# Performance work log

Hardware: AMD Instinct MI355X
Metric: run time of the kernel (lower is better)

## Reference

```python
import jax, jax.numpy as jnp
import numpy as np

N, E, F_IN, HID, NUM_CLASSES = 10000, 160000, 512, 1024, 100
NEG_SLOPE = 0.2  # PyG GATv2Conv default negative_slope


def setup_inputs() -> dict:
    key = jax.random.key(0)
    ks = jax.random.split(key, 10)
    return {
        "x": jax.random.normal(ks[0], (N, F_IN), jnp.float32),
        "edge_index": jax.random.randint(ks[1], (2, E), 0, N, dtype=jnp.int64)
        if jax.config.jax_enable_x64 else jax.random.randint(ks[1], (2, E), 0, N, dtype=jnp.int32),
        # GATv2Conv params (single head, out=1024): lin_l (source), lin_r (target), attention vector a, output bias
        "Wl": jax.random.normal(ks[2], (F_IN, HID), jnp.float32) / np.sqrt(F_IN),
        "bl": jnp.zeros((HID,), jnp.float32),
        "Wr": jax.random.normal(ks[3], (F_IN, HID), jnp.float32) / np.sqrt(F_IN),
        "br": jnp.zeros((HID,), jnp.float32),
        "att": jax.random.normal(ks[4], (HID,), jnp.float32) / np.sqrt(HID),
        "conv_b": jnp.zeros((HID,), jnp.float32),
        # MLP head: 1024 -> 512 -> 128 -> num_classes
        "W1": jax.random.normal(ks[5], (HID, 512), jnp.float32) / np.sqrt(HID),
        "b1": jnp.zeros((512,), jnp.float32),
        "W2": jax.random.normal(ks[6], (512, 128), jnp.float32) / np.sqrt(512),
        "b2": jnp.zeros((128,), jnp.float32),
        "Wc": jax.random.normal(ks[7], (128, NUM_CLASSES), jnp.float32) / np.sqrt(128),
        "bc": jnp.zeros((NUM_CLASSES,), jnp.float32),
    }


def _gatv2_conv(x, edge_index, Wl, bl, Wr, br, att, conv_b):
    """GATv2Conv, heads=1, add_self_loops=True, share_weights=False."""
    n = x.shape[0]
    loops = jnp.arange(n, dtype=edge_index.dtype)
    src = jnp.concatenate([edge_index[0], loops])  # message sources j
    dst = jnp.concatenate([edge_index[1], loops])  # message targets i
    xl = x @ Wl + bl  # [N, HID] source transform
    xr = x @ Wr + br  # [N, HID] target transform
    # e_ij = a^T LeakyReLU(xl_j + xr_i), per edge
    e = jax.nn.leaky_relu(xl[src] + xr[dst], negative_slope=NEG_SLOPE) @ att  # [E+N]
    # segment softmax over incoming edges of each target node (self-loops guarantee non-empty segments)
    m = jax.ops.segment_max(e, dst, num_segments=n)
    w = jnp.exp(e - m[dst])
    s = jax.ops.segment_sum(w, dst, num_segments=n)
    alpha = w / s[dst]  # [E+N]
    out = jax.ops.segment_sum(alpha[:, None] * xl[src], dst, num_segments=n)  # [N, HID]
    return out + conv_b


def reference(x, edge_index, Wl, bl, Wr, br, att, conv_b, W1, b1, W2, b2, Wc, bc):
    h = jax.nn.relu(_gatv2_conv(x, edge_index, Wl, bl, Wr, br, att, conv_b))
    h = jax.nn.relu(h @ W1 + b1)
    h = jax.nn.relu(h @ W2 + b2)
    return h @ Wc + bc
```

## Files before the change

### kernel.cpp

```cpp
#include <hip/hip_runtime.h>
#include <hip/hip_bf16.h>

constexpr int N_NODES = 10000;
constexpr int E_EDGES = 160000;
constexpr int F_IN    = 512;
constexpr int HID     = 1024;
constexpr int NCLS    = 100;
constexpr float NEG_SLOPE = 0.2f;

constexpr int BM = 128, BN = 128, BK = 32;
constexpr int M_PAD = ((N_NODES + BM - 1) / BM) * BM;

typedef __attribute__((ext_vector_type(8))) short bf16x8;
typedef __attribute__((ext_vector_type(4))) float f32x4;

__device__ inline void load_lds_16(const void* g, void* l) {
    __builtin_amdgcn_global_load_lds(
        (const __attribute__((address_space(1))) void*)g,
        (__attribute__((address_space(3))) void*)l, 16, 0, 0);
}

__device__ inline float bf2f(short s) {
    unsigned u = ((unsigned)(unsigned short)s) << 16;
    return __builtin_bit_cast(float, u);
}

__device__ inline float rfl(float x) {
    return __builtin_bit_cast(float,
        __builtin_amdgcn_readfirstlane(__builtin_bit_cast(int, x)));
}

__global__ __launch_bounds__(256) void gemm_mfma(
    const __hip_bfloat16* __restrict__ A, const __hip_bfloat16* __restrict__ Bt,
    const float* __restrict__ bias, int M, int K, int relu, int n_valid,
    __hip_bfloat16* __restrict__ Cb, int ldb, int m_blocks,
    const int* __restrict__ ei, int* __restrict__ cur, int* __restrict__ srcs)
{
    const int tid  = threadIdx.x;

    if ((int)blockIdx.y >= m_blocks) {
        int idx = ((blockIdx.y - m_blocks) * gridDim.x + blockIdx.x) * 256 + tid;
        if (idx < E_EDGES + N_NODES) {
            int s, d;
            if (idx < E_EDGES) { s = ei[idx]; d = ei[E_EDGES + idx]; }
            else               { s = idx - E_EDGES; d = s; }
            int p = atomicAdd(&cur[d], 1);
            srcs[p] = s;
        }
        return;
    }

    __shared__ __align__(16) short As[BM * BK];
    __shared__ __align__(16) short Bs[BN * BK];

    const int lane = tid & 63;
    const int w    = tid >> 6;
    const int m0   = blockIdx.y * BM;
    const int n0   = blockIdx.x * BN;

    f32x4 acc[4][4] = {};

    const int c0 = tid, c1 = tid + 256;
    const int r0 = c0 >> 2, cc0 = c0 & 3;
    const int r1 = c1 >> 2, cc1 = c1 & 3;

    const short* Ag0 = (const short*)A + (size_t)(m0 + r0) * K + cc0 * 8;
    const short* Ag1 = (const short*)A + (size_t)(m0 + r1) * K + cc1 * 8;
    const short* Bg0 = (const short*)Bt + (size_t)(n0 + r0) * K + cc0 * 8;
    const short* Bg1 = (const short*)Bt + (size_t)(n0 + r1) * K + cc1 * 8;

    const int wm = (w >> 1) * 64;
    const int wn = (w & 1) * 64;
    const int q  = lane >> 4;
    const int mr = lane & 15;

    for (int k0 = 0; k0 < K; k0 += BK) {
        __syncthreads();
        load_lds_16(Ag0 + k0, As + c0 * 8);
        load_lds_16(Ag1 + k0, As + c1 * 8);
        load_lds_16(Bg0 + k0, Bs + c0 * 8);
        load_lds_16(Bg1 + k0, Bs + c1 * 8);
        __syncthreads();

        bf16x8 af[4], bf[4];
        #pragma unroll
        for (int mt = 0; mt < 4; ++mt)
            af[mt] = *(const bf16x8*)&As[(wm + mt * 16 + mr) * BK + q * 8];
        #pragma unroll
        for (int nt = 0; nt < 4; ++nt)
            bf[nt] = *(const bf16x8*)&Bs[(wn + nt * 16 + mr) * BK + q * 8];
        #pragma unroll
        for (int mt = 0; mt < 4; ++mt)
            #pragma unroll
            for (int nt = 0; nt < 4; ++nt)
                acc[mt][nt] = __builtin_amdgcn_mfma_f32_16x16x32_bf16(
                    af[mt], bf[nt], acc[mt][nt], 0, 0, 0);
    }

    #pragma unroll
    for (int mt = 0; mt < 4; ++mt) {
        #pragma unroll
        for (int nt = 0; nt < 4; ++nt) {
            #pragma unroll
            for (int r = 0; r < 4; ++r) {
                int gm = m0 + wm + mt * 16 + q * 4 + r;
                int gn = n0 + wn + nt * 16 + mr;
                if (gm < M && gn < n_valid) {
                    float v = acc[mt][nt][r] + bias[gn];
                    if (relu) v = fmaxf(v, 0.f);
                    Cb[(size_t)gm * ldb + gn] = __float2bfloat16(v);
                }
            }
        }
    }
}

constexpr int HS_LD = 136;

__global__ __launch_bounds__(256) void mlp_tail(
    const __hip_bfloat16* __restrict__ h1, const __hip_bfloat16* __restrict__ W2t,
    const float* __restrict__ b2, const __hip_bfloat16* __restrict__ Wct,
    const float* __restrict__ bc, float* __restrict__ out)
{
    __shared__ __align__(16) short As[BM * BK];
    __shared__ __align__(16) short Bs[BN * BK];
    __shared__ __align__(16) short Hs[128 * HS_LD];

    const int tid  = threadIdx.x;
    const int lane = tid & 63;
    const int w    = tid >> 6;
    const int m0   = blockIdx.x * BM;

    const int c0 = tid, c1 = tid + 256;
    const int r0 = c0 >> 2, cc0 = c0 & 3;
    const int r1 = c1 >> 2, cc1 = c1 & 3;

    const int wm = (w >> 1) * 64;
    const int wn = (w & 1) * 64;
    const int q  = lane >> 4;
    const int mr = lane & 15;

    {
        f32x4 acc[4][4] = {};
        const short* Ag0 = (const short*)h1 + (size_t)(m0 + r0) * 512 + cc0 * 8;
        const short* Ag1 = (const short*)h1 + (size_t)(m0 + r1) * 512 + cc1 * 8;
        const short* Bg0 = (const short*)W2t + (size_t)r0 * 512 + cc0 * 8;
        const short* Bg1 = (const short*)W2t + (size_t)r1 * 512 + cc1 * 8;

        for (int k0 = 0; k0 < 512; k0 += BK) {
            __syncthreads();
            load_lds_16(Ag0 + k0, As + c0 * 8);
            load_lds_16(Ag1 + k0, As + c1 * 8);
            load_lds_16(Bg0 + k0, Bs + c0 * 8);
            load_lds_16(Bg1 + k0, Bs + c1 * 8);
            __syncthreads();

            bf16x8 af[4], bf[4];
            #pragma unroll
            for (int mt = 0; mt < 4; ++mt)
                af[mt] = *(const bf16x8*)&As[(wm + mt * 16 + mr) * BK + q * 8];
            #pragma unroll
            for (int nt = 0; nt < 4; ++nt)
                bf[nt] = *(const bf16x8*)&Bs[(wn + nt * 16 + mr) * BK + q * 8];
            #pragma unroll
            for (int mt = 0; mt < 4; ++mt)
                #pragma unroll
                for (int nt = 0; nt < 4; ++nt)
                    acc[mt][nt] = __builtin_amdgcn_mfma_f32_16x16x32_bf16(
                        af[mt], bf[nt], acc[mt][nt], 0, 0, 0);
        }
        #pragma unroll
        for (int mt = 0; mt < 4; ++mt)
            #pragma unroll
            for (int nt = 0; nt < 4; ++nt)
                #pragma unroll
                for (int r = 0; r < 4; ++r) {
                    int ml = wm + mt * 16 + q * 4 + r;
                    int nl = wn + nt * 16 + mr;
                    float v = fmaxf(acc[mt][nt][r] + b2[nl], 0.f);
                    Hs[ml * HS_LD + nl] =
                        __builtin_bit_cast(short, __float2bfloat16(v));
                }
    }

    {
        f32x4 acc[4][4] = {};
        const short* Bg0 = (const short*)Wct + (size_t)r0 * 128 + cc0 * 8;
        const short* Bg1 = (const short*)Wct + (size_t)r1 * 128 + cc1 * 8;

        for (int k0 = 0; k0 < 128; k0 += BK) {
            __syncthreads();
            load_lds_16(Bg0 + k0, Bs + c0 * 8);
            load_lds_16(Bg1 + k0, Bs + c1 * 8);
            __syncthreads();

            bf16x8 af[4], bf[4];
            #pragma unroll
            for (int mt = 0; mt < 4; ++mt)
                af[mt] = *(const bf16x8*)&Hs[(wm + mt * 16 + mr) * HS_LD + k0 + q * 8];
            #pragma unroll
            for (int nt = 0; nt < 4; ++nt)
                bf[nt] = *(const bf16x8*)&Bs[(wn + nt * 16 + mr) * BK + q * 8];
            #pragma unroll
            for (int mt = 0; mt < 4; ++mt)
                #pragma unroll
                for (int nt = 0; nt < 4; ++nt)
                    acc[mt][nt] = __builtin_amdgcn_mfma_f32_16x16x32_bf16(
                        af[mt], bf[nt], acc[mt][nt], 0, 0, 0);
        }
        #pragma unroll
        for (int mt = 0; mt < 4; ++mt)
            #pragma unroll
            for (int nt = 0; nt < 4; ++nt)
                #pragma unroll
                for (int r = 0; r < 4; ++r) {
                    int gm = m0 + wm + mt * 16 + q * 4 + r;
                    int gn = wn + nt * 16 + mr;
                    if (gm < N_NODES && gn < NCLS)
                        out[(size_t)gm * NCLS + gn] = acc[mt][nt][r] + bc[gn];
                }
    }
}

__device__ void transpose_tile(const float* __restrict__ W,
                               __hip_bfloat16* __restrict__ Wt,
                               int K, int N, int NP, int bx, int by,
                               int tx, int ty, float (*t)[33])
{
    int n0 = bx * 32, k0 = by * 32;
    #pragma unroll
    for (int i = 0; i < 32; i += 8) {
        int k = k0 + ty + i, n = n0 + tx;
        t[ty + i][tx] = (k < K && n < N) ? W[(size_t)k * N + n] : 0.f;
    }
    __syncthreads();
    #pragma unroll
    for (int i = 0; i < 32; i += 8) {
        int n = n0 + ty + i, k = k0 + tx;
        if (n < NP && k < K)
            Wt[(size_t)n * K + k] = __float2bfloat16(t[tx][ty + i]);
    }
}

constexpr int PK_X    = M_PAD * F_IN / 1024;
constexpr int PK_WL   = PK_X + 512;
constexpr int PK_WR   = PK_WL + 512;
constexpr int PK_W1   = PK_WR + 512;
constexpr int PK_W2   = PK_W1 + 64;
constexpr int PK_WC   = PK_W2 + 16;
constexpr int PK_BLR  = PK_WC + 8;
constexpr int PK_HIST = PK_BLR + (E_EDGES + 255) / 256;

__global__ __launch_bounds__(256) void pack_all(
    const float* __restrict__ x, __hip_bfloat16* __restrict__ xb,
    const float* __restrict__ Wl, const float* __restrict__ Wr,
    __hip_bfloat16* __restrict__ Wlrt,
    const float* __restrict__ W1, __hip_bfloat16* __restrict__ W1t,
    const float* __restrict__ W2, __hip_bfloat16* __restrict__ W2t,
    const float* __restrict__ Wc, __hip_bfloat16* __restrict__ Wct,
    const float* __restrict__ bl, const float* __restrict__ br,
    float* __restrict__ blr,
    const int* __restrict__ ei, int* __restrict__ deg)
{
    __shared__ float t[32][33];
    const int b = blockIdx.x;
    const int tid = threadIdx.x;
    const int tx = tid & 31, ty = tid >> 5;

    if (b < PK_X) {
        int i = b * 256 + tid;
        int row = i >> 7;
        int base = i << 2;
        short4 o;
        if (row < N_NODES) {
            const float4 v = *(const float4*)(x + base);
            o.x = __builtin_bit_cast(short, __float2bfloat16(v.x));
            o.y = __builtin_bit_cast(short, __float2bfloat16(v.y));
            o.z = __builtin_bit_cast(short, __float2bfloat16(v.z));
            o.w = __builtin_bit_cast(short, __float2bfloat16(v.w));
        } else {
            o.x = o.y = o.z = o.w = 0;
        }
        *(short4*)((short*)xb + base) = o;
    } else if (b < PK_WL) {
        int l = b - PK_X;
        transpose_tile(Wl, Wlrt, F_IN, HID, HID, l & 31, l >> 5, tx, ty, t);
    } else if (b < PK_WR) {
        int l = b - PK_WL;
        transpose_tile(Wr, Wlrt + (size_t)HID * F_IN, F_IN, HID, HID,
                       l & 31, l >> 5, tx, ty, t);
    } else if (b < PK_W1) {
        int l = b - PK_WR;
        transpose_tile(W1, W1t, HID, 512, 512, l & 15, l >> 4, tx, ty, t);
    } else if (b < PK_W2) {
        int l = b - PK_W1;
        transpose_tile(W2, W2t, 512, 128, 128, l & 3, l >> 2, tx, ty, t);
    } else if (b < PK_WC) {
        int l = b - PK_W2;
        transpose_tile(Wc, Wct, 128, NCLS, 128, l & 3, l >> 2, tx, ty, t);
    } else if (b < PK_BLR) {
        int i = (b - PK_WC) * 256 + tid;
        if (i < HID) blr[i] = bl[i];
        else if (i < 2 * HID) blr[i] = br[i - HID];
    } else {
        int e = (b - PK_BLR) * 256 + tid;
        if (e < E_EDGES) atomicAdd(&deg[ei[E_EDGES + e]], 1);
    }
}

__global__ __launch_bounds__(1024) void scan_deg(const int* __restrict__ deg,
                                                 int* __restrict__ off,
                                                 int* __restrict__ cur)
{
    __shared__ int tmp[1024];
    const int t = threadIdx.x;
    const int base = t * 10;
    int loc[10];
    int s = 0;
    #pragma unroll
    for (int j = 0; j < 10; ++j) {
        int n = base + j;
        loc[j] = s;
        s += (n < N_NODES) ? deg[n] + 1 : 0;
    }
    tmp[t] = s;
    __syncthreads();
    for (int st = 1; st < 1024; st <<= 1) {
        int add = (t >= st) ? tmp[t - st] : 0;
        __syncthreads();
        tmp[t] += add;
        __syncthreads();
    }
    const int excl = tmp[t] - s;
    #pragma unroll
    for (int j = 0; j < 10; ++j) {
        int n = base + j;
        if (n < N_NODES) { off[n] = excl + loc[j]; cur[n] = excl + loc[j]; }
    }
    if (t == 1023) off[N_NODES] = tmp[1023];
}

__global__ __launch_bounds__(256) void gat_node(
    const __hip_bfloat16* __restrict__ xlr, const float* __restrict__ att,
    const float* __restrict__ conv_b,
    const int* __restrict__ off, const int* __restrict__ srcs,
    __hip_bfloat16* __restrict__ h)
{
    const int tid  = threadIdx.x;
    const int lane = tid & 63;
    const int wave = tid >> 6;
    const int nloc = wave >> 1;
    const int wsub = wave & 1;
    const int i    = blockIdx.x * 2 + nloc;

    __shared__ float O_s[2][16 * 64];
    __shared__ float ml_s[2][2];

    const int beg  = off[i];
    const int end  = off[i + 1];
    const int last = end - 1;
    const short* base = (const short*)xlr;

    float xr_v[16], att_v[16];
    {
        const short* xri = base + (size_t)i * 2048 + HID + lane * 16;
        bf16x8 a0 = *(const bf16x8*)xri;
        bf16x8 a1 = *(const bf16x8*)(xri + 8);
        const float* ai = att + lane * 16;
        #pragma unroll
        for (int j = 0; j < 8; ++j) {
            xr_v[j] = bf2f(a0[j]);
            xr_v[8 + j] = bf2f(a1[j]);
        }
        #pragma unroll
        for (int j = 0; j < 16; ++j) att_v[j] = ai[j];
    }

    float m_w = -3e38f, l_w = 0.f;
    float O[16];
    #pragma unroll
    for (int j = 0; j < 16; ++j) O[j] = 0.f;

    int pos = beg + wsub;
    if (pos < end) {
        int sc = __builtin_amdgcn_readfirstlane(srcs[pos]);
        int sn = __builtin_amdgcn_readfirstlane(
                     srcs[pos + 2 <= last ? pos + 2 : last]);
        const short* rp = base + (size_t)sc * 2048 + lane * 16;
        bf16x8 a0 = *(const bf16x8*)rp;
        bf16x8 a1 = *(const bf16x8*)(rp + 8);

        for (; pos < end; pos += 2) {
            const short* np = base + (size_t)sn * 2048 + lane * 16;
            bf16x8 b0 = *(const bf16x8*)np;
            bf16x8 b1 = *(const bf16x8*)(np + 8);
            int s2 = srcs[pos + 4 <= last ? pos + 4 : last];

            float xf[16];
            #pragma unroll
            for (int j = 0; j < 8; ++j) {
                xf[j] = bf2f(a0[j]);
                xf[8 + j] = bf2f(a1[j]);
            }

            float p = 0.f;
            #pragma unroll
            for (int j = 0; j < 16; ++j) {
                float a = xf[j] + xr_v[j];
                a = fmaxf(a, NEG_SLOPE * a);
                p = __builtin_fmaf(att_v[j], a, p);
            }
            #pragma unroll
            for (int s = 1; s < 64; s <<= 1) p += __shfl_xor(p, s, 64);
            p = rfl(p);

            if (p > m_w) {
                const float scale = __expf(m_w - p);
                l_w = l_w * scale + 1.f;
                #pragma unroll
                for (int j = 0; j < 16; ++j) O[j] = O[j] * scale + xf[j];
                m_w = p;
            } else {
                const float alpha = __expf(p - m_w);
                l_w += alpha;
                #pragma unroll
                for (int j = 0; j < 16; ++j)
                    O[j] = __builtin_fmaf(alpha, xf[j], O[j]);
            }

            a0 = b0; a1 = b1;
            sn = __builtin_amdgcn_readfirstlane(s2);
        }
    }

    if (wsub == 1) {
        #pragma unroll
        for (int j = 0; j < 16; ++j) O_s[nloc][j * 64 + lane] = O[j];
        if (lane == 0) { ml_s[nloc][0] = m_w; ml_s[nloc][1] = l_w; }
    }
    __syncthreads();

    if (wsub == 0) {
        const float m1 = ml_s[nloc][0], l1 = ml_s[nloc][1];
        const float M  = fmaxf(m_w, m1);
        const float c0 = __expf(m_w - M);
        const float c1 = __expf(m1 - M);
        const float invL = 1.f / (l_w * c0 + l1 * c1);
        const float* cb = conv_b + lane * 16;
        bf16x8 o0, o1;
        #pragma unroll
        for (int j = 0; j < 8; ++j) {
            float r0 = __builtin_fmaf(
                c0 * O[j] + c1 * O_s[nloc][j * 64 + lane], invL, cb[j]);
            float r1 = __builtin_fmaf(
                c0 * O[8 + j] + c1 * O_s[nloc][(8 + j) * 64 + lane], invL,
                cb[8 + j]);
            r0 = fmaxf(r0, 0.f);
            r1 = fmaxf(r1, 0.f);
            o0[j] = __builtin_bit_cast(short, __float2bfloat16(r0));
            o1[j] = __builtin_bit_cast(short, __float2bfloat16(r1));
        }
        short* hp = (short*)h + (size_t)i * HID + lane * 16;
        *(bf16x8*)hp = o0;
        *(bf16x8*)(hp + 8) = o1;
    }
}

extern "C" void kernel_launch(void* const* d_in, const int* in_sizes, int n_in,
                              void* d_out, int out_size, void* d_ws, size_t ws_size,
                              hipStream_t stream)
{
    const float* x      = (const float*)d_in[0];
    const int*   ei     = (const int*)d_in[1];
    const float* Wl     = (const float*)d_in[2];
    const float* bl     = (const float*)d_in[3];
    const float* Wr     = (const float*)d_in[4];
    const float* br     = (const float*)d_in[5];
    const float* att    = (const float*)d_in[6];
    const float* conv_b = (const float*)d_in[7];
    const float* W1     = (const float*)d_in[8];
    const float* b1     = (const float*)d_in[9];
    const float* W2     = (const float*)d_in[10];
    const float* b2     = (const float*)d_in[11];
    const float* Wc     = (const float*)d_in[12];
    const float* bc     = (const float*)d_in[13];
    float* out = (float*)d_out;

    char* p = (char*)d_ws;
    __hip_bfloat16* xlr = (__hip_bfloat16*)p; p += (size_t)M_PAD * 2048 * 2;
    __hip_bfloat16* hb  = (__hip_bfloat16*)p; p += (size_t)M_PAD * HID * 2;
    __hip_bfloat16* xb  = (__hip_bfloat16*)p; p += (size_t)M_PAD * F_IN * 2;
    __hip_bfloat16* Wlrt= (__hip_bfloat16*)p; p += (size_t)2 * HID * F_IN * 2;
    __hip_bfloat16* W1t = (__hip_bfloat16*)p; p += (size_t)512 * HID * 2;
    __hip_bfloat16* W2t = (__hip_bfloat16*)p; p += (size_t)128 * 512 * 2;
    __hip_bfloat16* Wct = (__hip_bfloat16*)p; p += (size_t)128 * 128 * 2;
    float* blr = (float*)p;               p += 2 * HID * 4;
    int* deg  = (int*)p;                  p += N_NODES * 4;
    int* off  = (int*)p;                  p += (N_NODES + 1) * 4;
    int* cur  = (int*)p;                  p += N_NODES * 4;
    int* srcs = (int*)p;

    __hip_bfloat16* h1 = xb;

    const dim3 blk(256);

    hipMemsetAsync(deg, 0, N_NODES * sizeof(int), stream);

    pack_all<<<PK_HIST, blk, 0, stream>>>(x, xb, Wl, Wr, Wlrt, W1, W1t,
                                          W2, W2t, Wc, Wct, bl, br, blr,
                                          ei, deg);

    scan_deg<<<1, 1024, 0, stream>>>(deg, off, cur);

    constexpr int SCAT_Y = (E_EDGES + N_NODES + 16 * 256 - 1) / (16 * 256);
    gemm_mfma<<<dim3(2 * HID / BN, M_PAD / BM + SCAT_Y), blk, 0, stream>>>(
        xb, Wlrt, blr, N_NODES, F_IN, 0, 2 * HID, xlr, 2048,
        M_PAD / BM, ei, cur, srcs);

    gat_node<<<N_NODES / 2, blk, 0, stream>>>(xlr, att, conv_b, off, srcs, hb);

    gemm_mfma<<<dim3(512 / BN, M_PAD / BM), blk, 0, stream>>>(
        hb, W1t, b1, N_NODES, HID, 1, 512, h1, 512,
        M_PAD / BM, nullptr, nullptr, nullptr);

    mlp_tail<<<M_PAD / BM, blk, 0, stream>>>(h1, W2t, b2, Wct, bc, out);
}
```

Baseline: 277.8 us.

## Double-buffer LDS tiles, swizzle LDS layout, and vectorize GEMM epilogue stores

The main GEMM loop and the first stage of mlp_tail now use two LDS buffers. The next K-tile is prefetched with global_load_lds while the current tile feeds the MFMAs, which removes one barrier per iteration. The 16-byte chunk index in LDS is XOR-swizzled by row to cut bank conflicts on the fragment reads. The MFMA operands are swapped so each lane holds four consecutive columns, letting the epilogue write bias-added values as short4/float4 vector stores instead of scalar stores. With one barrier per iteration, correctness depends on the loads into the other buffer being ordered against the previous iteration's reads.

```diff
diff --git a/kernel.cpp b/kernel.cpp
--- a/kernel.cpp
+++ b/kernel.cpp
@@ -30,11 +30,25 @@
         __builtin_amdgcn_readfirstlane(__builtin_bit_cast(int, x)));
 }
 
+__device__ inline short4 cvt4(const f32x4 v, const float4 b, int relu) {
+    float r0 = v[0] + b.x, r1 = v[1] + b.y, r2 = v[2] + b.z, r3 = v[3] + b.w;
+    if (relu) {
+        r0 = fmaxf(r0, 0.f); r1 = fmaxf(r1, 0.f);
+        r2 = fmaxf(r2, 0.f); r3 = fmaxf(r3, 0.f);
+    }
+    short4 o;
+    o.x = __builtin_bit_cast(short, __float2bfloat16(r0));
+    o.y = __builtin_bit_cast(short, __float2bfloat16(r1));
+    o.z = __builtin_bit_cast(short, __float2bfloat16(r2));
+    o.w = __builtin_bit_cast(short, __float2bfloat16(r3));
+    return o;
+}
+
 __global__ __launch_bounds__(256) void gemm_mfma(
     const __hip_bfloat16* __restrict__ A, const __hip_bfloat16* __restrict__ Bt,
     const float* __restrict__ bias, int M, int K, int relu, int n_valid,
     __hip_bfloat16* __restrict__ Cb, int ldb, int m_blocks,
-    const int* __restrict__ ei, int* __restrict__ cur, int* __restrict__ srcs)
+    const int* __restrict__ ei, int* __restrict__ cur_, int* __restrict__ srcs)
 {
     const int tid  = threadIdx.x;
 
@@ -44,14 +58,14 @@
             int s, d;
             if (idx < E_EDGES) { s = ei[idx]; d = ei[E_EDGES + idx]; }
             else               { s = idx - E_EDGES; d = s; }
-            int p = atomicAdd(&cur[d], 1);
+            int p = atomicAdd(&cur_[d], 1);
             srcs[p] = s;
         }
         return;
     }
 
-    __shared__ __align__(16) short As[BM * BK];
-    __shared__ __align__(16) short Bs[BN * BK];
+    __shared__ __align__(16) short As[2][BM * BK];
+    __shared__ __align__(16) short Bs[2][BN * BK];
 
     const int lane = tid & 63;
     const int w    = tid >> 6;
@@ -61,8 +75,8 @@
     f32x4 acc[4][4] = {};
 
     const int c0 = tid, c1 = tid + 256;
-    const int r0 = c0 >> 2, cc0 = c0 & 3;
-    const int r1 = c1 >> 2, cc1 = c1 & 3;
+    const int r0 = c0 >> 2, cc0 = (c0 & 3) ^ ((r0 >> 2) & 3);
+    const int r1 = c1 >> 2, cc1 = (c1 & 3) ^ ((r1 >> 2) & 3);
 
     const short* Ag0 = (const short*)A + (size_t)(m0 + r0) * K + cc0 * 8;
     const short* Ag1 = (const short*)A + (size_t)(m0 + r1) * K + cc1 * 8;
@@ -73,44 +87,52 @@
     const int wn = (w & 1) * 64;
     const int q  = lane >> 4;
     const int mr = lane & 15;
-
+    const int sl = (q ^ (mr >> 2)) * 8;
+
+    load_lds_16(Ag0, As[0] + c0 * 8);
+    load_lds_16(Ag1, As[0] + c1 * 8);
+    load_lds_16(Bg0, Bs[0] + c0 * 8);
+    load_lds_16(Bg1, Bs[0] + c1 * 8);
+
+    int cur = 0;
     for (int k0 = 0; k0 < K; k0 += BK) {
         __syncthreads();
-        load_lds_16(Ag0 + k0, As + c0 * 8);
-        load_lds_16(Ag1 + k0, As + c1 * 8);
-        load_lds_16(Bg0 + k0, Bs + c0 * 8);
-        load_lds_16(Bg1 + k0, Bs + c1 * 8);
-        __syncthreads();
+        const int nxt = cur ^ 1;
+        const int kn = k0 + BK;
+        if (kn < K) {
+            load_lds_16(Ag0 + kn, As[nxt] + c0 * 8);
+            load_lds_16(Ag1 + kn, As[nxt] + c1 * 8);
+            load_lds_16(Bg0 + kn, Bs[nxt] + c0 * 8);
+            load_lds_16(Bg1 + kn, Bs[nxt] + c1 * 8);
+        }
 
         bf16x8 af[4], bf[4];
         #pragma unroll
         for (int mt = 0; mt < 4; ++mt)
-            af[mt] = *(const bf16x8*)&As[(wm + mt * 16 + mr) * BK + q * 8];
+            af[mt] = *(const bf16x8*)&As[cur][(wm + mt * 16 + mr) * BK + sl];
         #pragma unroll
         for (int nt = 0; nt < 4; ++nt)
-            bf[nt] = *(const bf16x8*)&Bs[(wn + nt * 16 + mr) * BK + q * 8];
+            bf[nt] = *(const bf16x8*)&Bs[cur][(wn + nt * 16 + mr) * BK + sl];
         #pragma unroll
         for (int mt = 0; mt < 4; ++mt)
             #pragma unroll
             for (int nt = 0; nt < 4; ++nt)
                 acc[mt][nt] = __builtin_amdgcn_mfma_f32_16x16x32_bf16(
-                    af[mt], bf[nt], acc[mt][nt], 0, 0, 0);
+                    bf[nt], af[mt], acc[mt][nt], 0, 0, 0);
+        cur = nxt;
     }
 
     #pragma unroll
     for (int mt = 0; mt < 4; ++mt) {
+        const int gm = m0 + wm + mt * 16 + mr;
+        if (gm >= M) continue;
         #pragma unroll
         for (int nt = 0; nt < 4; ++nt) {
-            #pragma unroll
-            for (int r = 0; r < 4; ++r) {
-                int gm = m0 + wm + mt * 16 + q * 4 + r;
-                int gn = n0 + wn + nt * 16 + mr;
-                if (gm < M && gn < n_valid) {
-                    float v = acc[mt][nt][r] + bias[gn];
-                    if (relu) v = fmaxf(v, 0.f);
-                    Cb[(size_t)gm * ldb + gn] = __float2bfloat16(v);
-                }
-            }
+            const int gn = n0 + wn + nt * 16 + q * 4;
+            if (gn >= n_valid) continue;
+            const float4 bv = *(const float4*)&bias[gn];
+            short4 o = cvt4(acc[mt][nt], bv, relu);
+            *(short4*)((short*)Cb + (size_t)gm * ldb + gn) = o;
         }
     }
 }
@@ -122,8 +144,8 @@
     const float* __restrict__ b2, const __hip_bfloat16* __restrict__ Wct,
     const float* __restrict__ bc, float* __restrict__ out)
 {
-    __shared__ __align__(16) short As[BM * BK];
-    __shared__ __align__(16) short Bs[BN * BK];
+    __shared__ __align__(16) short As[2][BM * BK];
+    __shared__ __align__(16) short Bs[2][BN * BK];
     __shared__ __align__(16) short Hs[128 * HS_LD];
 
     const int tid  = threadIdx.x;
@@ -132,13 +154,14 @@
     const int m0   = blockIdx.x * BM;
 
     const int c0 = tid, c1 = tid + 256;
-    const int r0 = c0 >> 2, cc0 = c0 & 3;
-    const int r1 = c1 >> 2, cc1 = c1 & 3;
+    const int r0 = c0 >> 2, cc0 = (c0 & 3) ^ ((r0 >> 2) & 3);
+    const int r1 = c1 >> 2, cc1 = (c1 & 3) ^ ((r1 >> 2) & 3);
 
     const int wm = (w >> 1) * 64;
     const int wn = (w & 1) * 64;
     const int q  = lane >> 4;
     const int mr = lane & 15;
+    const int sl = (q ^ (mr >> 2)) * 8;
 
     {
         f32x4 acc[4][4] = {};
@@ -147,40 +170,49 @@
         const short* Bg0 = (const short*)W2t + (size_t)r0 * 512 + cc0 * 8;
         const short* Bg1 = (const short*)W2t + (size_t)r1 * 512 + cc1 * 8;
 
+        load_lds_16(Ag0, As[0] + c0 * 8);
+        load_lds_16(Ag1, As[0] + c1 * 8);
+        load_lds_16(Bg0, Bs[0] + c0 * 8);
+        load_lds_16(Bg1, Bs[0] + c1 * 8);
+
+        int cur = 0;
         for (int k0 = 0; k0 < 512; k0 += BK) {
             __syncthreads();
-            load_lds_16(Ag0 + k0, As + c0 * 8);
-            load_lds_16(Ag1 + k0, As + c1 * 8);
-            load_lds_16(Bg0 + k0, Bs + c0 * 8);
-            load_lds_16(Bg1 + k0, Bs + c1 * 8);
-            __syncthreads();
-
+            const int nxt = cur ^ 1;
+            const int kn = k0 + BK;
+            if (kn < 512) {
+                load_lds_16(Ag0 + kn, As[nxt] + c0 * 8);
+                load_lds_16(Ag1 + kn, As[nxt] + c1 * 8);
+                load_lds_16(Bg0 + kn, Bs[nxt] + c0 * 8);
+                load_lds_16(Bg1 + kn, Bs[nxt] + c1 * 8);
+            }
             bf16x8 af[4], bf[4];
             #pragma unroll
             for (int mt = 0; mt < 4; ++mt)
-                af[mt] = *(const bf16x8*)&As[(wm + mt * 16 + mr) * BK + q * 8];
+                af[mt] = *(const bf16x8*)&As[cur][(wm + mt * 16 + mr) * BK + sl];
             #pragma unroll
             for (int nt = 0; nt < 4; ++nt)
-                bf[nt] = *(const bf16x8*)&Bs[(wn + nt * 16 + mr) * BK + q * 8];
+                bf[nt] = *(const bf16x8*)&Bs[cur][(wn + nt * 16 + mr) * BK + sl];
             #pragma unroll
             for (int mt = 0; mt < 4; ++mt)
                 #pragma unroll
                 for (int nt = 0; nt < 4; ++nt)
                     acc[mt][nt] = __builtin_amdgcn_mfma_f32_16x16x32_bf16(
-                        af[mt], bf[nt], acc[mt][nt], 0, 0, 0);
-        }
-        #pragma unroll
-        for (int mt = 0; mt < 4; ++mt)
-            #pragma unroll
-            for (int nt = 0; nt < 4; ++nt)
-                #pragma unroll
-                for (int r = 0; r < 4; ++r) {
-                    int ml = wm + mt * 16 + q * 4 + r;
-                    int nl = wn + nt * 16 + mr;
-                    float v = fmaxf(acc[mt][nt][r] + b2[nl], 0.f);
-                    Hs[ml * HS_LD + nl] =
-                        __builtin_bit_cast(short, __float2bfloat16(v));
-                }
+                        bf[nt], af[mt], acc[mt][nt], 0, 0, 0);
+            cur = nxt;
+        }
+        __syncthreads();
+        #pragma unroll
+        for (int mt = 0; mt < 4; ++mt) {
+            const int ml = wm + mt * 16 + mr;
+            #pragma unroll
+            for (int nt = 0; nt < 4; ++nt) {
+                const int nl = wn + nt * 16 + q * 4;
+                const float4 bv = *(const float4*)&b2[nl];
+                short4 o = cvt4(acc[mt][nt], bv, 1);
+                *(short4*)&Hs[ml * HS_LD + nl] = o;
+            }
+        }
     }
 
     {
@@ -190,8 +222,8 @@
 
         for (int k0 = 0; k0 < 128; k0 += BK) {
             __syncthreads();
-            load_lds_16(Bg0 + k0, Bs + c0 * 8);
-            load_lds_16(Bg1 + k0, Bs + c1 * 8);
+            load_lds_16(Bg0 + k0, Bs[0] + c0 * 8);
+            load_lds_16(Bg1 + k0, Bs[0] + c1 * 8);
             __syncthreads();
 
             bf16x8 af[4], bf[4];
@@ -200,25 +232,31 @@
                 af[mt] = *(const bf16x8*)&Hs[(wm + mt * 16 + mr) * HS_LD + k0 + q * 8];
             #pragma unroll
             for (int nt = 0; nt < 4; ++nt)
-                bf[nt] = *(const bf16x8*)&Bs[(wn + nt * 16 + mr) * BK + q * 8];
+                bf[nt] = *(const bf16x8*)&Bs[0][(wn + nt * 16 + mr) * BK + sl];
             #pragma unroll
             for (int mt = 0; mt < 4; ++mt)
                 #pragma unroll
                 for (int nt = 0; nt < 4; ++nt)
                     acc[mt][nt] = __builtin_amdgcn_mfma_f32_16x16x32_bf16(
-                        af[mt], bf[nt], acc[mt][nt], 0, 0, 0);
-        }
-        #pragma unroll
-        for (int mt = 0; mt < 4; ++mt)
-            #pragma unroll
-            for (int nt = 0; nt < 4; ++nt)
-                #pragma unroll
-                for (int r = 0; r < 4; ++r) {
-                    int gm = m0 + wm + mt * 16 + q * 4 + r;
-                    int gn = wn + nt * 16 + mr;
-                    if (gm < N_NODES && gn < NCLS)
-                        out[(size_t)gm * NCLS + gn] = acc[mt][nt][r] + bc[gn];
-                }
+                        bf[nt], af[mt], acc[mt][nt], 0, 0, 0);
+        }
+        #pragma unroll
+        for (int mt = 0; mt < 4; ++mt) {
+            const int gm = m0 + wm + mt * 16 + mr;
+            if (gm >= N_NODES) continue;
+            #pragma unroll
+            for (int nt = 0; nt < 4; ++nt) {
+                const int gn = wn + nt * 16 + q * 4;
+                if (gn >= NCLS) continue;
+                const float4 bv = *(const float4*)&bc[gn];
+                float4 o;
+                o.x = acc[mt][nt][0] + bv.x;
+                o.y = acc[mt][nt][1] + bv.y;
+                o.z = acc[mt][nt][2] + bv.z;
+                o.w = acc[mt][nt][3] + bv.w;
+                *(float4*)(out + (size_t)gm * NCLS + gn) = o;
+            }
+        }
     }
 }
 
```

Result: faster. 257.9 us (-7.2%).
